# Kernel optimization log

Hardware: AMD Instinct MI355X
Metric: run time of the kernel (lower is better)

## Reference

```python
import jax, jax.numpy as jnp
import numpy as np

B, T, C, H, HD = 2, 2048, 768, 12, 64  # batch, seq, n_embd, n_head, head_dim
D2 = HD // 2
FF = 4 * C
EPS = 1e-5


def setup_inputs() -> dict:
    key = jax.random.key(0)
    ks = jax.random.split(key, 8)
    s = 0.02  # init scale for weights
    # realistic RoPE cos/sin tables over half the head dim
    pos = jnp.arange(T, dtype=jnp.float32)[:, None]                     # [T,1]
    inv_freq = 1.0 / (10000.0 ** (jnp.arange(D2, dtype=jnp.float32) / D2))
    ang = pos * inv_freq                                                # [T,D2]
    return {
        "x": jax.random.normal(ks[0], (B, T, C), jnp.float32),
        "cos": jnp.cos(ang)[None, :, None, :],                          # [1,T,1,D2]
        "sin": jnp.sin(ang)[None, :, None, :],
        "wq": jax.random.normal(ks[1], (C, C), jnp.float32) * s,        # Linear, bias=False ([in,out])
        "wk": jax.random.normal(ks[2], (C, C), jnp.float32) * s,
        "wv": jax.random.normal(ks[3], (C, C), jnp.float32) * s,
        "wo": jax.random.normal(ks[4], (C, C), jnp.float32) * s,
        "wfc": jax.random.normal(ks[5], (C, FF), jnp.float32) * s,
        "wpr": jax.random.normal(ks[6], (FF, C), jnp.float32) * s,
        "g1": jnp.ones((C,), jnp.float32),
        "g2": jnp.ones((C,), jnp.float32),
    }


def _rmsnorm(x, g):
    return g * (x * jax.lax.rsqrt(jnp.mean(x * x, axis=-1, keepdims=True) + EPS))


def _rope(x, cos, sin):
    # x: [B,T,H,HD]; half-split RoPE as in apply_rotary_emb
    x1, x2 = x[..., :D2], x[..., D2:]
    return jnp.concatenate([x1 * cos + x2 * sin, -x1 * sin + x2 * cos], axis=-1)


def reference(x, cos, sin, wq, wk, wv, wo, wfc, wpr, g1, g2):
    # --- attention sublayer ---
    h = _rmsnorm(x, g1)
    q = (h @ wq).reshape(B, T, H, HD)
    k = (h @ wk).reshape(B, T, H, HD)
    v = (h @ wv).reshape(B, T, H, HD)
    q = _rope(q, cos, sin)
    k = _rope(k, cos, sin)
    scale = 1.0 / np.sqrt(HD).astype(np.float32)
    att = jnp.einsum('bqhd,bkhd->bhqk', q, k) * scale                   # [B,H,T,T]
    causal = jnp.tril(jnp.ones((T, T), dtype=bool))
    att = jnp.where(causal[None, None], att, -jnp.inf)
    p = jax.nn.softmax(att, axis=-1)
    y = jnp.einsum('bhqk,bkhd->bqhd', p, v).reshape(B, T, C)
    x = x + y @ wo
    # --- MLP sublayer: ReLU^2 ---
    h2 = _rmsnorm(x, g2)
    x = x + jnp.square(jax.nn.relu(h2 @ wfc)) @ wpr
    return x
```

## Files before the change

### kernel.cpp

```cpp
#include <hip/hip_runtime.h>
#include <hip/hip_bf16.h>
#include <math.h>

#define Bn 2
#define Tn 2048
#define Cn 768
#define Hn 12
#define HDn 64
#define D2n 32
#define FFn 3072
#define EPSn 1e-5f
#define QKVS (3 * Cn)

typedef short s16x8 __attribute__((ext_vector_type(8)));
typedef float f32x4 __attribute__((ext_vector_type(4)));
typedef unsigned short u16;

__device__ __forceinline__ u16 f2bf(float f) {
    union { float f; unsigned u; } v;
    v.f = f;
    unsigned r = (v.u + 0x7fffu + ((v.u >> 16) & 1u)) >> 16;
    return (u16)r;
}
__device__ __forceinline__ float bf2f(u16 u) {
    union { unsigned u; float f; } v;
    v.u = ((unsigned)u) << 16;
    return v.f;
}
__device__ __forceinline__ unsigned pack2(float a, float b) {
    union { float f; unsigned u; } va, vb;
    va.f = a; vb.f = b;
    return (va.u >> 16) | (vb.u & 0xffff0000u);
}

__device__ __forceinline__ void gl2lds16(const void* g, void* l) {
    __builtin_amdgcn_global_load_lds((const __attribute__((address_space(1))) void*)g,
                                     (__attribute__((address_space(3))) void*)l,
                                     16, 0, 0);
}

__global__ __launch_bounds__(256) void rmsnorm_bf16_kernel(const float* __restrict__ x,
                                                           const float* __restrict__ g,
                                                           u16* __restrict__ out) {
    int row = blockIdx.x;
    const float* xr = x + (size_t)row * Cn;
    u16* orow = out + (size_t)row * Cn;
    int tid = threadIdx.x;
    float v[3];
    float ss = 0.f;
#pragma unroll
    for (int i = 0; i < 3; ++i) {
        v[i] = xr[tid + 256 * i];
        ss += v[i] * v[i];
    }
#pragma unroll
    for (int o = 32; o; o >>= 1) ss += __shfl_xor(ss, o);
    __shared__ float red[4];
    int w = tid >> 6;
    if ((tid & 63) == 0) red[w] = ss;
    __syncthreads();
    float tot = red[0] + red[1] + red[2] + red[3];
    float s = rsqrtf(tot / (float)Cn + EPSn);
#pragma unroll
    for (int i = 0; i < 3; ++i) {
        int c = tid + 256 * i;
        orow[c] = f2bf(g[c] * v[i] * s);
    }
}

__global__ __launch_bounds__(256) void reduce2_rmsnorm_kernel(const float* __restrict__ p0,
                                                              const float* __restrict__ p1,
                                                              const float* __restrict__ x,
                                                              const float* __restrict__ g,
                                                              float* __restrict__ x1,
                                                              u16* __restrict__ h2) {
    int row = blockIdx.x;
    size_t base = (size_t)row * Cn;
    int tid = threadIdx.x;
    float v[3];
    float ss = 0.f;
#pragma unroll
    for (int i = 0; i < 3; ++i) {
        size_t c = base + tid + 256 * i;
        float t = x[c] + p0[c] + p1[c];
        v[i] = t;
        ss += t * t;
    }
#pragma unroll
    for (int o = 32; o; o >>= 1) ss += __shfl_xor(ss, o);
    __shared__ float red[4];
    int w = tid >> 6;
    if ((tid & 63) == 0) red[w] = ss;
    __syncthreads();
    float tot = red[0] + red[1] + red[2] + red[3];
    float s = rsqrtf(tot / (float)Cn + EPSn);
#pragma unroll
    for (int i = 0; i < 3; ++i) {
        int c = tid + 256 * i;
        x1[base + c] = v[i];
        h2[base + c] = f2bf(g[c] * v[i] * s);
    }
}

__global__ __launch_bounds__(256) void reduce_final_kernel(const float* __restrict__ q0,
                                                           const float* __restrict__ qrest,
                                                           const float* __restrict__ x1,
                                                           float* __restrict__ out) {
    const size_t MN = (size_t)Bn * Tn * Cn;
    size_t i = ((size_t)blockIdx.x * 256 + threadIdx.x) * 4;
    float4 a = *(const float4*)&x1[i];
    float4 b = *(const float4*)&q0[i];
    float4 c = *(const float4*)&qrest[i];
    float4 d = *(const float4*)&qrest[MN + i];
    float4 r;
    r.x = a.x + b.x + c.x + d.x;
    r.y = a.y + b.y + c.y + d.y;
    r.z = a.z + b.z + c.z + d.z;
    r.w = a.w + b.w + c.w + d.w;
    *(float4*)&out[i] = r;
}

__global__ __launch_bounds__(256) void transpose_bf16_kernel(const float* __restrict__ W,
                                                             u16* __restrict__ Wt,
                                                             int K, int N) {
    __shared__ u16 t[32][33];
    int bx = blockIdx.x * 32;
    int by = blockIdx.y * 32;
    int tx = threadIdx.x & 31, ty = threadIdx.x >> 5;
#pragma unroll
    for (int i = 0; i < 4; ++i) {
        int kk = by + ty + i * 8;
        t[ty + i * 8][tx] = f2bf(W[(size_t)kk * N + bx + tx]);
    }
    __syncthreads();
#pragma unroll
    for (int i = 0; i < 4; ++i) {
        int n = bx + ty + i * 8;
        Wt[(size_t)n * K + by + tx] = t[tx][ty + i * 8];
    }
}

template <int EPI, int NI>
__global__ __launch_bounds__(256) void gemm_bt(const u16* __restrict__ A,
                                               const u16* __restrict__ Bt,
                                               const float* __restrict__ R,
                                               void* __restrict__ Cout,
                                               int M, int N, int K) {
    __shared__ u16 As[128 * 32];
    __shared__ u16 Bs[NI * 32 * 32];
    int tid = threadIdx.x;
    int w = tid >> 6, lane = tid & 63;
    int quad = lane >> 4, l16 = lane & 15;
    int bm = blockIdx.y * 128;
    int bn = blockIdx.x * (NI * 32);
    int wrow = (w & 1) * 64, wcol = (w >> 1) * (NI * 16);

    f32x4 acc[4][NI];
#pragma unroll
    for (int i = 0; i < 4; ++i)
#pragma unroll
        for (int j = 0; j < NI; ++j) acc[i][j] = (f32x4){0.f, 0.f, 0.f, 0.f};

    int srow = lane >> 2;
    int scol = (lane & 3) * 8;

    for (int k0 = 0; k0 < K; k0 += 32) {
        __syncthreads();
#pragma unroll
        for (int r = 0; r < 2; ++r) {
            int row = r * 64 + w * 16 + srow;
            gl2lds16(A + (size_t)(bm + row) * K + k0 + scol, &As[(r * 64 + w * 16) * 32]);
        }
#pragma unroll
        for (int r = 0; r < NI / 2; ++r) {
            int row = r * 64 + w * 16 + srow;
            gl2lds16(Bt + (size_t)(bn + row) * K + k0 + scol, &Bs[(r * 64 + w * 16) * 32]);
        }
        __syncthreads();

        s16x8 af[4], bf[NI];
#pragma unroll
        for (int mi = 0; mi < 4; ++mi)
            af[mi] = *(const s16x8*)&As[(wrow + mi * 16 + l16) * 32 + quad * 8];
#pragma unroll
        for (int ni = 0; ni < NI; ++ni)
            bf[ni] = *(const s16x8*)&Bs[(wcol + ni * 16 + l16) * 32 + quad * 8];
#pragma unroll
        for (int mi = 0; mi < 4; ++mi)
#pragma unroll
            for (int ni = 0; ni < NI; ++ni)
                acc[mi][ni] = __builtin_amdgcn_mfma_f32_16x16x32_bf16(af[mi], bf[ni],
                                                                      acc[mi][ni], 0, 0, 0);
    }

#pragma unroll
    for (int mi = 0; mi < 4; ++mi) {
#pragma unroll
        for (int rg = 0; rg < 4; ++rg) {
            size_t row = bm + wrow + mi * 16 + quad * 4 + rg;
#pragma unroll
            for (int ni = 0; ni < NI; ++ni) {
                size_t idx = row * N + bn + wcol + ni * 16 + l16;
                float c = acc[mi][ni][rg];
                if (EPI == 0) {
                    ((float*)Cout)[idx] = c;
                } else if (EPI == 1) {
                    ((float*)Cout)[idx] = c + R[idx];
                } else if (EPI == 2) {
                    c = fmaxf(c, 0.f);
                    ((u16*)Cout)[idx] = f2bf(c * c);
                } else {
                    ((u16*)Cout)[idx] = f2bf(c);
                }
            }
        }
    }
}

template <int NI>
__global__ __launch_bounds__(256) void gemm_bt_part(const u16* __restrict__ A,
                                                    const u16* __restrict__ Bt,
                                                    float* __restrict__ P,
                                                    int M, int N, int lda,
                                                    int Kc, int kidx0) {
    __shared__ u16 As[128 * 32];
    __shared__ u16 Bs[NI * 32 * 32];
    int tid = threadIdx.x;
    int w = tid >> 6, lane = tid & 63;
    int quad = lane >> 4, l16 = lane & 15;
    int bm = blockIdx.y * 128;
    int bn = blockIdx.x * (NI * 32);
    int wrow = (w & 1) * 64, wcol = (w >> 1) * (NI * 16);
    int kbase = (kidx0 + blockIdx.z) * Kc;

    f32x4 acc[4][NI];
#pragma unroll
    for (int i = 0; i < 4; ++i)
#pragma unroll
        for (int j = 0; j < NI; ++j) acc[i][j] = (f32x4){0.f, 0.f, 0.f, 0.f};

    int srow = lane >> 2;
    int scol = (lane & 3) * 8;

    for (int k0 = 0; k0 < Kc; k0 += 32) {
        __syncthreads();
#pragma unroll
        for (int r = 0; r < 2; ++r) {
            int row = r * 64 + w * 16 + srow;
            gl2lds16(A + (size_t)(bm + row) * lda + kbase + k0 + scol,
                     &As[(r * 64 + w * 16) * 32]);
        }
#pragma unroll
        for (int r = 0; r < NI / 2; ++r) {
            int row = r * 64 + w * 16 + srow;
            gl2lds16(Bt + (size_t)(bn + row) * lda + kbase + k0 + scol,
                     &Bs[(r * 64 + w * 16) * 32]);
        }
        __syncthreads();

        s16x8 af[4], bf[NI];
#pragma unroll
        for (int mi = 0; mi < 4; ++mi)
            af[mi] = *(const s16x8*)&As[(wrow + mi * 16 + l16) * 32 + quad * 8];
#pragma unroll
        for (int ni = 0; ni < NI; ++ni)
            bf[ni] = *(const s16x8*)&Bs[(wcol + ni * 16 + l16) * 32 + quad * 8];
#pragma unroll
        for (int mi = 0; mi < 4; ++mi)
#pragma unroll
            for (int ni = 0; ni < NI; ++ni)
                acc[mi][ni] = __builtin_amdgcn_mfma_f32_16x16x32_bf16(af[mi], bf[ni],
                                                                      acc[mi][ni], 0, 0, 0);
    }

    float* Pz = P + (size_t)blockIdx.z * M * N;
#pragma unroll
    for (int mi = 0; mi < 4; ++mi) {
#pragma unroll
        for (int rg = 0; rg < 4; ++rg) {
            size_t row = bm + wrow + mi * 16 + quad * 4 + rg;
#pragma unroll
            for (int ni = 0; ni < NI; ++ni)
                Pz[row * N + bn + wcol + ni * 16 + l16] = acc[mi][ni][rg];
        }
    }
}

__global__ __launch_bounds__(256) void rope_prep_kernel(const u16* __restrict__ qkvb,
                                                        const float* __restrict__ cosp,
                                                        const float* __restrict__ sinp,
                                                        u16* __restrict__ qh,
                                                        u16* __restrict__ kh,
                                                        u16* __restrict__ vtp) {
    __shared__ u16 sT[64][72];
    int tc = blockIdx.x, bh = blockIdx.y;
    int h = bh % Hn, b = bh / Hn;
    int t0 = tc * 64;
    int tid = threadIdx.x;

    int r = tid >> 2;
    int c = (tid & 3) * 8;
    int t = t0 + r;
    size_t srow = (size_t)(b * Tn + t) * QKVS + h * HDn;
    float4 c0 = *(const float4*)&cosp[t * D2n + c];
    float4 c1 = *(const float4*)&cosp[t * D2n + c + 4];
    float4 s0 = *(const float4*)&sinp[t * D2n + c];
    float4 s1 = *(const float4*)&sinp[t * D2n + c + 4];
    float cs[8] = {c0.x, c0.y, c0.z, c0.w, c1.x, c1.y, c1.z, c1.w};
    float sn[8] = {s0.x, s0.y, s0.z, s0.w, s1.x, s1.y, s1.z, s1.w};
#pragma unroll
    for (int tens = 0; tens < 2; ++tens) {
        size_t off = srow + tens * Cn;
        float sc = tens ? 1.f : 0.125f;
        ushort4 lo0 = *(const ushort4*)&qkvb[off + c];
        ushort4 lo1 = *(const ushort4*)&qkvb[off + c + 4];
        ushort4 hi0 = *(const ushort4*)&qkvb[off + c + 32];
        ushort4 hi1 = *(const ushort4*)&qkvb[off + c + 36];
        u16 lo[8] = {lo0.x, lo0.y, lo0.z, lo0.w, lo1.x, lo1.y, lo1.z, lo1.w};
        u16 hi[8] = {hi0.x, hi0.y, hi0.z, hi0.w, hi1.x, hi1.y, hi1.z, hi1.w};
        u16 o1[8], o2[8];
#pragma unroll
        for (int j = 0; j < 8; ++j) {
            float x1 = bf2f(lo[j]), x2 = bf2f(hi[j]);
            o1[j] = f2bf((x1 * cs[j] + x2 * sn[j]) * sc);
            o2[j] = f2bf((-x1 * sn[j] + x2 * cs[j]) * sc);
        }
        u16* dst = (tens ? kh : qh) + ((size_t)bh * Tn + t) * HDn;
        *(ushort4*)&dst[c]      = make_ushort4(o1[0], o1[1], o1[2], o1[3]);
        *(ushort4*)&dst[c + 4]  = make_ushort4(o1[4], o1[5], o1[6], o1[7]);
        *(ushort4*)&dst[c + 32] = make_ushort4(o2[0], o2[1], o2[2], o2[3]);
        *(ushort4*)&dst[c + 36] = make_ushort4(o2[4], o2[5], o2[6], o2[7]);
    }

    int r2 = tid >> 2;
    int cc = (tid & 3) * 16;
    size_t vrow = (size_t)(b * Tn + t0 + r2) * QKVS + h * HDn + 2 * Cn;
#pragma unroll
    for (int j = 0; j < 4; ++j)
        *(ushort4*)&sT[r2][cc + j * 4] = *(const ushort4*)&qkvb[vrow + cc + j * 4];
    __syncthreads();
    int d = tid >> 2;
#pragma unroll
    for (int p = 0; p < 2; ++p) {
        int s = (tid & 3) + p * 4;
        int h2 = s >> 2, qq = s & 3;
        u16 e[8];
#pragma unroll
        for (int j = 0; j < 4; ++j) e[j] = sT[32 * h2 + qq * 4 + j][d];
#pragma unroll
        for (int j = 0; j < 4; ++j) e[4 + j] = sT[32 * h2 + 16 + qq * 4 + j][d];
        size_t outb = ((size_t)bh * HDn + d) * Tn + t0 + s * 8;
        *(ushort4*)&vtp[outb]     = make_ushort4(e[0], e[1], e[2], e[3]);
        *(ushort4*)&vtp[outb + 4] = make_ushort4(e[4], e[5], e[6], e[7]);
    }
}

#define APAD 72

__global__ __launch_bounds__(256) void attn_v3_kernel(const u16* __restrict__ qh,
                                                      const u16* __restrict__ kh,
                                                      const u16* __restrict__ vtp,
                                                      u16* __restrict__ y) {
    __shared__ u16 sQ[64 * APAD];
    __shared__ u16 sK[64 * APAD];
    __shared__ u16 sVp[64 * APAD];

    int qt = 31 - (blockIdx.x / 24);
    int bh = blockIdx.x % 24;
    int h = bh % Hn, b = bh / Hn;
    int qbase = qt * 64;
    int tid = threadIdx.x;
    int lane = tid & 63, w = tid >> 6;
    int quad = lane >> 4, l16 = lane & 15;

    const u16* qg = qh + (size_t)bh * Tn * HDn;
    const u16* kg = kh + (size_t)bh * Tn * HDn;
    const u16* vg = vtp + (size_t)bh * HDn * Tn;

#pragma unroll
    for (int i = 0; i < 2; ++i) {
        int idx = tid + 256 * i;
        int row = idx >> 3, blk = idx & 7;
        *(s16x8*)&sQ[row * APAD + blk * 8] =
            *(const s16x8*)&qg[(size_t)(qbase + row) * HDn + blk * 8];
    }
    __syncthreads();

    s16x8 qf0 = *(const s16x8*)&sQ[(w * 16 + l16) * APAD + quad * 8];
    s16x8 qf1 = *(const s16x8*)&sQ[(w * 16 + l16) * APAD + 32 + quad * 8];

    f32x4 acc[4];
#pragma unroll
    for (int i = 0; i < 4; ++i) acc[i] = (f32x4){0.f, 0.f, 0.f, 0.f};
    float m = -3e38f, l = 0.f;
    const int qloc = w * 16 + l16;

    for (int kbase = 0; kbase <= qbase; kbase += 64) {
        __syncthreads();
#pragma unroll
        for (int i = 0; i < 2; ++i) {
            int idx = tid + 256 * i;
            int row = idx >> 3, blk = idx & 7;
            *(s16x8*)&sK[row * APAD + blk * 8] =
                *(const s16x8*)&kg[(size_t)(kbase + row) * HDn + blk * 8];
            *(s16x8*)&sVp[row * APAD + blk * 8] =
                *(const s16x8*)&vg[(size_t)row * Tn + kbase + blk * 8];
        }
        __syncthreads();

        const bool diag = (kbase == qbase);

        f32x4 st[4];
#pragma unroll
        for (int kb = 0; kb < 4; ++kb) {
            s16x8 kf0 = *(const s16x8*)&sK[(kb * 16 + l16) * APAD + quad * 8];
            s16x8 kf1 = *(const s16x8*)&sK[(kb * 16 + l16) * APAD + 32 + quad * 8];
            f32x4 cfr = (f32x4){0.f, 0.f, 0.f, 0.f};
            cfr = __builtin_amdgcn_mfma_f32_16x16x32_bf16(kf0, qf0, cfr, 0, 0, 0);
            cfr = __builtin_amdgcn_mfma_f32_16x16x32_bf16(kf1, qf1, cfr, 0, 0, 0);
            st[kb] = cfr;
        }

        if (diag) {
#pragma unroll
            for (int kb = 0; kb < 4; ++kb)
#pragma unroll
                for (int rg = 0; rg < 4; ++rg)
                    if (kb * 16 + quad * 4 + rg > qloc) st[kb][rg] = -1e30f;
        }

        float mx = -3e38f;
#pragma unroll
        for (int kb = 0; kb < 4; ++kb)
#pragma unroll
            for (int rg = 0; rg < 4; ++rg) mx = fmaxf(mx, st[kb][rg]);
        mx = fmaxf(mx, __shfl_xor(mx, 16));
        mx = fmaxf(mx, __shfl_xor(mx, 32));
        float mnew = fmaxf(m, mx);
        float alpha = __expf(m - mnew);
        m = mnew;
        float tsum = 0.f;
#pragma unroll
        for (int kb = 0; kb < 4; ++kb) {
#pragma unroll
            for (int rg = 0; rg < 4; ++rg) {
                float p = __expf(st[kb][rg] - mnew);
                st[kb][rg] = p;
                tsum += p;
            }
        }
        tsum += __shfl_xor(tsum, 16);
        tsum += __shfl_xor(tsum, 32);
        l = l * alpha + tsum;

        float aq[4];
#pragma unroll
        for (int rg = 0; rg < 4; ++rg) aq[rg] = __shfl(alpha, quad * 4 + rg);
#pragma unroll
        for (int db = 0; db < 4; ++db)
#pragma unroll
            for (int rg = 0; rg < 4; ++rg) acc[db][rg] *= aq[rg];

        union { s16x8 v; unsigned u[4]; } pa0, pa1;
        pa0.u[0] = pack2(st[0][0], st[0][1]);
        pa0.u[1] = pack2(st[0][2], st[0][3]);
        pa0.u[2] = pack2(st[1][0], st[1][1]);
        pa0.u[3] = pack2(st[1][2], st[1][3]);
        pa1.u[0] = pack2(st[2][0], st[2][1]);
        pa1.u[1] = pack2(st[2][2], st[2][3]);
        pa1.u[2] = pack2(st[3][0], st[3][1]);
        pa1.u[3] = pack2(st[3][2], st[3][3]);

#pragma unroll
        for (int db = 0; db < 4; ++db) {
            int rr = db * 16 + l16;
            s16x8 vf0 = *(const s16x8*)&sVp[rr * APAD + quad * 8];
            s16x8 vf1 = *(const s16x8*)&sVp[rr * APAD + 32 + quad * 8];
            acc[db] = __builtin_amdgcn_mfma_f32_16x16x32_bf16(pa0.v, vf0, acc[db], 0, 0, 0);
            acc[db] = __builtin_amdgcn_mfma_f32_16x16x32_bf16(pa1.v, vf1, acc[db], 0, 0, 0);
        }
    }

    float lq[4];
#pragma unroll
    for (int rg = 0; rg < 4; ++rg) lq[rg] = __shfl(l, quad * 4 + rg);
#pragma unroll
    for (int db = 0; db < 4; ++db) {
#pragma unroll
        for (int rg = 0; rg < 4; ++rg) {
            int row = qbase + w * 16 + quad * 4 + rg;
            y[((size_t)(b * Tn + row) * Hn + h) * HDn + db * 16 + l16] =
                f2bf(acc[db][rg] / lq[rg]);
        }
    }
}

extern "C" void kernel_launch(void* const* d_in, const int* in_sizes, int n_in,
                              void* d_out, int out_size, void* d_ws, size_t ws_size,
                              hipStream_t stream) {
    const float* x    = (const float*)d_in[0];
    const float* cosp = (const float*)d_in[1];
    const float* sinp = (const float*)d_in[2];
    const float* wq   = (const float*)d_in[3];
    const float* wk   = (const float*)d_in[4];
    const float* wv   = (const float*)d_in[5];
    const float* wo   = (const float*)d_in[6];
    const float* wfc  = (const float*)d_in[7];
    const float* wpr  = (const float*)d_in[8];
    const float* g1   = (const float*)d_in[9];
    const float* g2   = (const float*)d_in[10];
    float* out = (float*)d_out;

    const size_t S = (size_t)Bn * Tn * Cn;
    const size_t MN = S;
    char* W = (char*)d_ws;
    u16* slotA = (u16*)W;
    u16* qkvb  = (u16*)(W + 2 * S);
    u16* yh    = (u16*)(W + 2 * S);
    float* wop = (float*)(W + 4 * S);
    u16* fbuf  = (u16*)(W + 4 * S);
    u16* qhb   = (u16*)(W + 8 * S);
    u16* khb   = (u16*)(W + 10 * S);
    u16* vtpb  = (u16*)(W + 12 * S);
    float* x1  = (float*)(W + 14 * S);
    u16* wt_qkv = (u16*)(W + 18 * S);
    u16* wt_o   = wt_qkv + (size_t)QKVS * Cn;
    u16* wt_fc  = wt_o + (size_t)Cn * Cn;
    u16* wt_pr  = wt_fc + (size_t)FFn * Cn;
    const size_t WB = ((size_t)QKVS * Cn + (size_t)Cn * Cn + 2 * (size_t)FFn * Cn) * 2;
    float* q0    = (float*)W;
    float* qrest = (float*)(W + 18 * S + WB);

    const int M = Bn * Tn;

    transpose_bf16_kernel<<<dim3(Cn / 32, Cn / 32), 256, 0, stream>>>(wq, wt_qkv, Cn, Cn);
    transpose_bf16_kernel<<<dim3(Cn / 32, Cn / 32), 256, 0, stream>>>(wk, wt_qkv + (size_t)Cn * Cn, Cn, Cn);
    transpose_bf16_kernel<<<dim3(Cn / 32, Cn / 32), 256, 0, stream>>>(wv, wt_qkv + (size_t)2 * Cn * Cn, Cn, Cn);
    transpose_bf16_kernel<<<dim3(Cn / 32, Cn / 32), 256, 0, stream>>>(wo, wt_o, Cn, Cn);
    transpose_bf16_kernel<<<dim3(FFn / 32, Cn / 32), 256, 0, stream>>>(wfc, wt_fc, Cn, FFn);
    transpose_bf16_kernel<<<dim3(Cn / 32, FFn / 32), 256, 0, stream>>>(wpr, wt_pr, FFn, Cn);

    rmsnorm_bf16_kernel<<<M, 256, 0, stream>>>(x, g1, slotA);

    gemm_bt<3, 4><<<dim3(QKVS / 128, M / 128), 256, 0, stream>>>(slotA, wt_qkv, nullptr,
                                                                 qkvb, M, QKVS, Cn);

    rope_prep_kernel<<<dim3(Tn / 64, Bn * Hn), 256, 0, stream>>>(qkvb, cosp, sinp,
                                                                 qhb, khb, vtpb);

    attn_v3_kernel<<<Bn * Hn * (Tn / 64), 256, 0, stream>>>(qhb, khb, vtpb, yh);

    gemm_bt_part<2><<<dim3(Cn / 64, M / 128, 2), 256, 0, stream>>>(yh, wt_o, wop,
                                                                   M, Cn, Cn, Cn / 2, 0);
    reduce2_rmsnorm_kernel<<<M, 256, 0, stream>>>(wop, wop + MN, x, g2, x1, slotA);

    gemm_bt<2, 4><<<dim3(FFn / 128, M / 128), 256, 0, stream>>>(slotA, wt_fc, nullptr,
                                                                fbuf, M, FFn, Cn);

    gemm_bt_part<2><<<dim3(Cn / 64, M / 128, 1), 256, 0, stream>>>(fbuf, wt_pr, q0,
                                                                   M, Cn, FFn, FFn / 3, 0);
    gemm_bt_part<2><<<dim3(Cn / 64, M / 128, 2), 256, 0, stream>>>(fbuf, wt_pr, qrest,
                                                                   M, Cn, FFn, FFn / 3, 1);

    reduce_final_kernel<<<(int)(MN / 1024), 256, 0, stream>>>(q0, qrest, x1, out);
}
```

Measured before the change: 309.2 us.

## Widen attention key tiles to 128, swizzle LDS, use exp2, merge weight transposes

```diff
diff --git a/kernel.cpp b/kernel.cpp
--- a/kernel.cpp
+++ b/kernel.cpp
@@ -11,6 +11,7 @@
 #define FFn 3072
 #define EPSn 1e-5f
 #define QKVS (3 * Cn)
+#define LOG2E 1.4426950408889634f
 
 typedef short s16x8 __attribute__((ext_vector_type(8)));
 typedef float f32x4 __attribute__((ext_vector_type(4)));
@@ -120,12 +121,31 @@
     *(float4*)&out[i] = r;
 }
 
-__global__ __launch_bounds__(256) void transpose_bf16_kernel(const float* __restrict__ W,
-                                                             u16* __restrict__ Wt,
-                                                             int K, int N) {
+__global__ __launch_bounds__(256) void transpose_all_kernel(const float* __restrict__ wq,
+                                                            const float* __restrict__ wk,
+                                                            const float* __restrict__ wv,
+                                                            const float* __restrict__ wo,
+                                                            const float* __restrict__ wfc,
+                                                            const float* __restrict__ wpr,
+                                                            u16* __restrict__ wt_qkv,
+                                                            u16* __restrict__ wt_o,
+                                                            u16* __restrict__ wt_fc,
+                                                            u16* __restrict__ wt_pr) {
+    int id = blockIdx.x;
+    const float* W;
+    u16* Wt;
+    int K, N, lid;
+    if (id < 576)       { W = wq;  Wt = wt_qkv;                      K = Cn;  N = Cn;  lid = id; }
+    else if (id < 1152) { W = wk;  Wt = wt_qkv + (size_t)Cn * Cn;    K = Cn;  N = Cn;  lid = id - 576; }
+    else if (id < 1728) { W = wv;  Wt = wt_qkv + (size_t)2 * Cn * Cn;K = Cn;  N = Cn;  lid = id - 1152; }
+    else if (id < 2304) { W = wo;  Wt = wt_o;                        K = Cn;  N = Cn;  lid = id - 1728; }
+    else if (id < 4608) { W = wfc; Wt = wt_fc;                       K = Cn;  N = FFn; lid = id - 2304; }
+    else                { W = wpr; Wt = wt_pr;                       K = FFn; N = Cn;  lid = id - 4608; }
+    int ntx = N / 32;
+    int bx = (lid % ntx) * 32;
+    int by = (lid / ntx) * 32;
+
     __shared__ u16 t[32][33];
-    int bx = blockIdx.x * 32;
-    int by = blockIdx.y * 32;
     int tx = threadIdx.x & 31, ty = threadIdx.x >> 5;
 #pragma unroll
     for (int i = 0; i < 4; ++i) {
@@ -311,7 +331,7 @@
 #pragma unroll
     for (int tens = 0; tens < 2; ++tens) {
         size_t off = srow + tens * Cn;
-        float sc = tens ? 1.f : 0.125f;
+        float sc = tens ? 1.f : (0.125f * LOG2E);
         ushort4 lo0 = *(const ushort4*)&qkvb[off + c];
         ushort4 lo1 = *(const ushort4*)&qkvb[off + c + 4];
         ushort4 hi0 = *(const ushort4*)&qkvb[off + c + 32];
@@ -355,15 +375,13 @@
     }
 }
 
-#define APAD 72
-
-__global__ __launch_bounds__(256) void attn_v3_kernel(const u16* __restrict__ qh,
+__global__ __launch_bounds__(256) void attn_v4_kernel(const u16* __restrict__ qh,
                                                       const u16* __restrict__ kh,
                                                       const u16* __restrict__ vtp,
                                                       u16* __restrict__ y) {
-    __shared__ u16 sQ[64 * APAD];
-    __shared__ u16 sK[64 * APAD];
-    __shared__ u16 sVp[64 * APAD];
+    __shared__ u16 sQ[64 * 64];
+    __shared__ u16 sK[128 * 64];
+    __shared__ u16 sV[64 * 128];
 
     int qt = 31 - (blockIdx.x / 24);
     int bh = blockIdx.x % 24;
@@ -379,15 +397,16 @@
 
 #pragma unroll
     for (int i = 0; i < 2; ++i) {
-        int idx = tid + 256 * i;
-        int row = idx >> 3, blk = idx & 7;
-        *(s16x8*)&sQ[row * APAD + blk * 8] =
-            *(const s16x8*)&qg[(size_t)(qbase + row) * HDn + blk * 8];
+        int id = tid + 256 * i;
+        int row = id >> 3, bd = id & 7;
+        *(s16x8*)&sQ[row * 64 + ((bd ^ (row & 7)) * 8)] =
+            *(const s16x8*)&qg[(size_t)(qbase + row) * HDn + bd * 8];
     }
     __syncthreads();
 
-    s16x8 qf0 = *(const s16x8*)&sQ[(w * 16 + l16) * APAD + quad * 8];
-    s16x8 qf1 = *(const s16x8*)&sQ[(w * 16 + l16) * APAD + 32 + quad * 8];
+    const int sw = l16 & 7;
+    s16x8 qf0 = *(const s16x8*)&sQ[(w * 16 + l16) * 64 + ((quad ^ sw) * 8)];
+    s16x8 qf1 = *(const s16x8*)&sQ[(w * 16 + l16) * 64 + (((quad + 4) ^ sw) * 8)];
 
     f32x4 acc[4];
 #pragma unroll
@@ -395,56 +414,61 @@
     float m = -3e38f, l = 0.f;
     const int qloc = w * 16 + l16;
 
-    for (int kbase = 0; kbase <= qbase; kbase += 64) {
+    for (int kbase = 0; kbase <= qbase; kbase += 128) {
         __syncthreads();
 #pragma unroll
-        for (int i = 0; i < 2; ++i) {
-            int idx = tid + 256 * i;
-            int row = idx >> 3, blk = idx & 7;
-            *(s16x8*)&sK[row * APAD + blk * 8] =
-                *(const s16x8*)&kg[(size_t)(kbase + row) * HDn + blk * 8];
-            *(s16x8*)&sVp[row * APAD + blk * 8] =
-                *(const s16x8*)&vg[(size_t)row * Tn + kbase + blk * 8];
+        for (int i = 0; i < 4; ++i) {
+            int id = tid + 256 * i;
+            int row = id >> 3, bd = id & 7;
+            *(s16x8*)&sK[row * 64 + ((bd ^ (row & 7)) * 8)] =
+                *(const s16x8*)&kg[(size_t)(kbase + row) * HDn + bd * 8];
+        }
+#pragma unroll
+        for (int i = 0; i < 4; ++i) {
+            int id = tid + 256 * i;
+            int row = id >> 4, c = id & 15;
+            *(s16x8*)&sV[row * 128 + (((c & 8) | ((c & 7) ^ (row & 7))) * 8)] =
+                *(const s16x8*)&vg[(size_t)row * Tn + kbase + c * 8];
         }
         __syncthreads();
 
-        const bool diag = (kbase == qbase);
-
-        f32x4 st[4];
-#pragma unroll
-        for (int kb = 0; kb < 4; ++kb) {
-            s16x8 kf0 = *(const s16x8*)&sK[(kb * 16 + l16) * APAD + quad * 8];
-            s16x8 kf1 = *(const s16x8*)&sK[(kb * 16 + l16) * APAD + 32 + quad * 8];
+        f32x4 st[8];
+#pragma unroll
+        for (int kb = 0; kb < 8; ++kb) {
+            int row = kb * 16 + l16;
+            s16x8 kf0 = *(const s16x8*)&sK[row * 64 + ((quad ^ sw) * 8)];
+            s16x8 kf1 = *(const s16x8*)&sK[row * 64 + (((quad + 4) ^ sw) * 8)];
             f32x4 cfr = (f32x4){0.f, 0.f, 0.f, 0.f};
             cfr = __builtin_amdgcn_mfma_f32_16x16x32_bf16(kf0, qf0, cfr, 0, 0, 0);
             cfr = __builtin_amdgcn_mfma_f32_16x16x32_bf16(kf1, qf1, cfr, 0, 0, 0);
             st[kb] = cfr;
         }
 
-        if (diag) {
-#pragma unroll
-            for (int kb = 0; kb < 4; ++kb)
+        if (kbase + 128 > qbase) {
+            int qlim = qbase - kbase + qloc;
+#pragma unroll
+            for (int kb = 0; kb < 8; ++kb)
 #pragma unroll
                 for (int rg = 0; rg < 4; ++rg)
-                    if (kb * 16 + quad * 4 + rg > qloc) st[kb][rg] = -1e30f;
+                    if (kb * 16 + quad * 4 + rg > qlim) st[kb][rg] = -1e30f;
         }
 
         float mx = -3e38f;
 #pragma unroll
-        for (int kb = 0; kb < 4; ++kb)
+        for (int kb = 0; kb < 8; ++kb)
 #pragma unroll
             for (int rg = 0; rg < 4; ++rg) mx = fmaxf(mx, st[kb][rg]);
         mx = fmaxf(mx, __shfl_xor(mx, 16));
         mx = fmaxf(mx, __shfl_xor(mx, 32));
         float mnew = fmaxf(m, mx);
-        float alpha = __expf(m - mnew);
+        float alpha = exp2f(m - mnew);
         m = mnew;
         float tsum = 0.f;
 #pragma unroll
-        for (int kb = 0; kb < 4; ++kb) {
+        for (int kb = 0; kb < 8; ++kb) {
 #pragma unroll
             for (int rg = 0; rg < 4; ++rg) {
-                float p = __expf(st[kb][rg] - mnew);
+                float p = exp2f(st[kb][rg] - mnew);
                 st[kb][rg] = p;
                 tsum += p;
             }
@@ -461,23 +485,27 @@
 #pragma unroll
             for (int rg = 0; rg < 4; ++rg) acc[db][rg] *= aq[rg];
 
-        union { s16x8 v; unsigned u[4]; } pa0, pa1;
-        pa0.u[0] = pack2(st[0][0], st[0][1]);
-        pa0.u[1] = pack2(st[0][2], st[0][3]);
-        pa0.u[2] = pack2(st[1][0], st[1][1]);
-        pa0.u[3] = pack2(st[1][2], st[1][3]);
-        pa1.u[0] = pack2(st[2][0], st[2][1]);
-        pa1.u[1] = pack2(st[2][2], st[2][3]);
-        pa1.u[2] = pack2(st[3][0], st[3][1]);
-        pa1.u[3] = pack2(st[3][2], st[3][3]);
+        union { s16x8 v; unsigned u[4]; } pa[4];
+#pragma unroll
+        for (int t = 0; t < 4; ++t) {
+            pa[t].u[0] = pack2(st[2 * t][0], st[2 * t][1]);
+            pa[t].u[1] = pack2(st[2 * t][2], st[2 * t][3]);
+            pa[t].u[2] = pack2(st[2 * t + 1][0], st[2 * t + 1][1]);
+            pa[t].u[3] = pack2(st[2 * t + 1][2], st[2 * t + 1][3]);
+        }
 
 #pragma unroll
         for (int db = 0; db < 4; ++db) {
             int rr = db * 16 + l16;
-            s16x8 vf0 = *(const s16x8*)&sVp[rr * APAD + quad * 8];
-            s16x8 vf1 = *(const s16x8*)&sVp[rr * APAD + 32 + quad * 8];
-            acc[db] = __builtin_amdgcn_mfma_f32_16x16x32_bf16(pa0.v, vf0, acc[db], 0, 0, 0);
-            acc[db] = __builtin_amdgcn_mfma_f32_16x16x32_bf16(pa1.v, vf1, acc[db], 0, 0, 0);
+#pragma unroll
+            for (int hf = 0; hf < 2; ++hf) {
+                int c0 = hf * 8 + quad;
+                int c1 = hf * 8 + quad + 4;
+                s16x8 vf0 = *(const s16x8*)&sV[rr * 128 + (((c0 & 8) | ((c0 & 7) ^ sw)) * 8)];
+                s16x8 vf1 = *(const s16x8*)&sV[rr * 128 + (((c1 & 8) | ((c1 & 7) ^ sw)) * 8)];
+                acc[db] = __builtin_amdgcn_mfma_f32_16x16x32_bf16(pa[2 * hf].v, vf0, acc[db], 0, 0, 0);
+                acc[db] = __builtin_amdgcn_mfma_f32_16x16x32_bf16(pa[2 * hf + 1].v, vf1, acc[db], 0, 0, 0);
+            }
         }
     }
 
@@ -533,12 +561,8 @@
 
     const int M = Bn * Tn;
 
-    transpose_bf16_kernel<<<dim3(Cn / 32, Cn / 32), 256, 0, stream>>>(wq, wt_qkv, Cn, Cn);
-    transpose_bf16_kernel<<<dim3(Cn / 32, Cn / 32), 256, 0, stream>>>(wk, wt_qkv + (size_t)Cn * Cn, Cn, Cn);
-    transpose_bf16_kernel<<<dim3(Cn / 32, Cn / 32), 256, 0, stream>>>(wv, wt_qkv + (size_t)2 * Cn * Cn, Cn, Cn);
-    transpose_bf16_kernel<<<dim3(Cn / 32, Cn / 32), 256, 0, stream>>>(wo, wt_o, Cn, Cn);
-    transpose_bf16_kernel<<<dim3(FFn / 32, Cn / 32), 256, 0, stream>>>(wfc, wt_fc, Cn, FFn);
-    transpose_bf16_kernel<<<dim3(Cn / 32, FFn / 32), 256, 0, stream>>>(wpr, wt_pr, FFn, Cn);
+    transpose_all_kernel<<<6912, 256, 0, stream>>>(wq, wk, wv, wo, wfc, wpr,
+                                                   wt_qkv, wt_o, wt_fc, wt_pr);
 
     rmsnorm_bf16_kernel<<<M, 256, 0, stream>>>(x, g1, slotA);
 
@@ -548,7 +572,7 @@
     rope_prep_kernel<<<dim3(Tn / 64, Bn * Hn), 256, 0, stream>>>(qkvb, cosp, sinp,
                                                                  qhb, khb, vtpb);
 
-    attn_v3_kernel<<<Bn * Hn * (Tn / 64), 256, 0, stream>>>(qhb, khb, vtpb, yh);
+    attn_v4_kernel<<<Bn * Hn * (Tn / 64), 256, 0, stream>>>(qhb, khb, vtpb, yh);
 
     gemm_bt_part<2><<<dim3(Cn / 64, M / 128, 2), 256, 0, stream>>>(yh, wt_o, wop,
                                                                    M, Cn, Cn, Cn / 2, 0);
```

Result: faster. 294.9 us (-4.6%).
